# Kernel optimization log

Measured on AMD Instinct MI355X. Metric: run time of the kernel, lower is better.

## Reference

```python
import jax, jax.numpy as jnp
import numpy as np

B, S, N = 16, 512, 8          # batch, sentence length, num hash functions
M_BLOOM = 4096                # bloom filter length
W_WIN = 2                     # moving-window half width


def setup_inputs() -> dict:
    key = jax.random.key(0)
    hashes = jax.random.randint(key, (B, S, N), 0, 2147483647, dtype=jnp.int32)
    return {"hashes": hashes}


def counting_bloom(hashes, m):
    # hashes: [B, S, N] int -> counts [B, M, S] float32 (per-position histogram of N hashes mod m)
    b, s, _ = hashes.shape
    fp = jnp.remainder(hashes, m)
    counts = jnp.zeros((b, s, m), jnp.float32).at[
        jnp.arange(b)[:, None, None], jnp.arange(s)[None, :, None], fp
    ].add(1.0)
    return jnp.transpose(counts, (0, 2, 1))  # [B, M, S]


def moving_window(fc, w):
    # fc: [B, M, S] -> [B, (2w+1)*M, S]; block k holds fc shifted right by (w-k) along S, zero-padded
    _, _, s = fc.shape
    blocks = []
    for k in range(2 * w + 1):
        sh = w - k  # positive = shift right, negative = shift left
        if sh > 0:
            blk = jnp.pad(fc[:, :, : s - sh], ((0, 0), (0, 0), (sh, 0)))
        elif sh < 0:
            blk = jnp.pad(fc[:, :, -sh:], ((0, 0), (0, 0), (0, -sh)))
        else:
            blk = fc
        blocks.append(blk)
    return jnp.concatenate(blocks, axis=1)


def reference(hashes):
    fc = counting_bloom(hashes, M_BLOOM)      # [B, M, S]
    return moving_window(fc, W_WIN)           # [B, (2W+1)*M, S]
```

## Files before the change

kernel.cpp:

```cpp
#include <hip/hip_runtime.h>

#define B_DIM 16
#define S_DIM 512
#define N_HASH 8
#define M_BLOOM 4096
#define W_WIN 2
#define K_BLOCKS (2 * W_WIN + 1)
#define OUT_ELEMS (B_DIM * K_BLOCKS * M_BLOOM * S_DIM)

typedef float fx4 __attribute__((ext_vector_type(4)));

__global__ void zero_out_kernel(fx4* __restrict__ out, int n4) {
    const fx4 z = {0.0f, 0.0f, 0.0f, 0.0f};
    int idx = blockIdx.x * blockDim.x + threadIdx.x;
    const int stride = gridDim.x * blockDim.x;
    for (int i = idx; i < n4; i += stride) {
        out[i] = z;
    }
}

__global__ void scatter_kernel(const int* __restrict__ hashes,
                               float* __restrict__ out) {
    int idx = blockIdx.x * blockDim.x + threadIdx.x;
    if (idx >= B_DIM * S_DIM * N_HASH) return;

    const int b = idx / (S_DIM * N_HASH);
    const int s = (idx / N_HASH) % S_DIM;

    const int h = hashes[idx];
    const int m = h & (M_BLOOM - 1);

    const long long base_bm = ((long long)b * K_BLOCKS) * M_BLOOM + m;
#pragma unroll
    for (int k = 0; k < K_BLOCKS; ++k) {
        const int s_out = s + (W_WIN - k);
        if (s_out >= 0 && s_out < S_DIM) {
            const long long off =
                (base_bm + (long long)k * M_BLOOM) * S_DIM + s_out;
            atomicAdd(out + off, 1.0f);
        }
    }
}

extern "C" void kernel_launch(void* const* d_in, const int* in_sizes, int n_in,
                              void* d_out, int out_size, void* d_ws, size_t ws_size,
                              hipStream_t stream) {
    const int* hashes = (const int*)d_in[0];
    float* out = (float*)d_out;

    const int n4 = OUT_ELEMS / 4;
    zero_out_kernel<<<8192, 256, 0, stream>>>((fx4*)out, n4);

    const int total_hashes = B_DIM * S_DIM * N_HASH;
    scatter_kernel<<<(total_hashes + 255) / 256, 256, 0, stream>>>(hashes, out);
}
```

Before: 706.3 us.

## Fuse zeroing and atomic scatter into LDS histogram tile with dense shifted writes

Replaces the separate zero-fill kernel and the global atomicAdd scatter with one kernel. Each block owns one batch and a 64-row slice of the bloom dimension. It builds byte-sized counts in a padded LDS tile, then writes all five shifted window blocks as dense, coalesced float4 stores. This removes the extra full-output write pass and the scattered global atomics. In exchange, every block rereads the batch's hashes and does unaligned byte-extraction work in LDS.

```diff
diff --git a/kernel.cpp b/kernel.cpp
--- a/kernel.cpp
+++ b/kernel.cpp
@@ -1,4 +1,5 @@
 #include <hip/hip_runtime.h>
+#include <stdint.h>
 
 #define B_DIM 16
 #define S_DIM 512
@@ -8,37 +9,67 @@
 #define K_BLOCKS (2 * W_WIN + 1)
 #define OUT_ELEMS (B_DIM * K_BLOCKS * M_BLOOM * S_DIM)
 
+#define M_CHUNK 64
+#define TILE_STRIDE 520
+#define TILE_BYTES (M_CHUNK * TILE_STRIDE)
+
 typedef float fx4 __attribute__((ext_vector_type(4)));
 
-__global__ void zero_out_kernel(fx4* __restrict__ out, int n4) {
-    const fx4 z = {0.0f, 0.0f, 0.0f, 0.0f};
-    int idx = blockIdx.x * blockDim.x + threadIdx.x;
-    const int stride = gridDim.x * blockDim.x;
-    for (int i = idx; i < n4; i += stride) {
-        out[i] = z;
+__global__ __launch_bounds__(256) void bloom_window_kernel(
+    const int* __restrict__ hashes, float* __restrict__ out) {
+    __shared__ uint32_t tile32[TILE_BYTES / 4];
+    uint8_t* tile = (uint8_t*)tile32;
+
+    const int tid = threadIdx.x;
+    const int b = blockIdx.x >> 6;
+    const int chunk = blockIdx.x & 63;
+    const int m0 = chunk * M_CHUNK;
+
+    for (int i = tid; i < TILE_BYTES / 4; i += 256) tile32[i] = 0;
+    __syncthreads();
+
+    const int4* hp = (const int4*)hashes;
+#pragma unroll
+    for (int ss = 0; ss < 2; ++ss) {
+        const int s = 2 * tid + ss;
+        const int4 h01 = hp[(b * S_DIM + s) * 2 + 0];
+        const int4 h23 = hp[(b * S_DIM + s) * 2 + 1];
+        const int hv[8] = {h01.x, h01.y, h01.z, h01.w,
+                           h23.x, h23.y, h23.z, h23.w};
+#pragma unroll
+        for (int n = 0; n < N_HASH; ++n) {
+            const int m = hv[n] & (M_BLOOM - 1);
+            const unsigned ml = (unsigned)(m - m0);
+            if (ml < M_CHUNK) {
+                tile[ml * TILE_STRIDE + 4 + s] += 1;
+            }
+        }
     }
-}
+    __syncthreads();
 
-__global__ void scatter_kernel(const int* __restrict__ hashes,
-                               float* __restrict__ out) {
-    int idx = blockIdx.x * blockDim.x + threadIdx.x;
-    if (idx >= B_DIM * S_DIM * N_HASH) return;
+    fx4* out4 = (fx4*)out;
+    const int n_items = K_BLOCKS * M_CHUNK * (S_DIM / 4);
+    for (int idx = tid; idx < n_items; idx += 256) {
+        const int j = idx & 127;
+        const int r = idx >> 7;
+        const int k = r >> 6;
+        const int m = r & 63;
 
-    const int b = idx / (S_DIM * N_HASH);
-    const int s = (idx / N_HASH) % S_DIM;
+        const int base = m * TILE_STRIDE + 4 + 4 * j + (k - 2);
+        const uint32_t* wp = (const uint32_t*)(tile + (base & ~3));
+        const uint32_t lo = wp[0];
+        const uint32_t hi = wp[1];
+        const uint32_t sh = (uint32_t)(base & 3) * 8u;
+        const uint32_t packed = sh ? ((lo >> sh) | (hi << (32u - sh))) : lo;
 
-    const int h = hashes[idx];
-    const int m = h & (M_BLOOM - 1);
+        fx4 v;
+        v.x = (float)(packed & 0xffu);
+        v.y = (float)((packed >> 8) & 0xffu);
+        v.z = (float)((packed >> 16) & 0xffu);
+        v.w = (float)((packed >> 24) & 0xffu);
 
-    const long long base_bm = ((long long)b * K_BLOCKS) * M_BLOOM + m;
-#pragma unroll
-    for (int k = 0; k < K_BLOCKS; ++k) {
-        const int s_out = s + (W_WIN - k);
-        if (s_out >= 0 && s_out < S_DIM) {
-            const long long off =
-                (base_bm + (long long)k * M_BLOOM) * S_DIM + s_out;
-            atomicAdd(out + off, 1.0f);
-        }
+        const int row = (b * K_BLOCKS + k) * M_BLOOM + m0 + m;
+        out4[(long long)row * (S_DIM / 4) + j] = v;
     }
 }
 
@@ -48,9 +79,5 @@
     const int* hashes = (const int*)d_in[0];
     float* out = (float*)d_out;
 
-    const int n4 = OUT_ELEMS / 4;
-    zero_out_kernel<<<8192, 256, 0, stream>>>((fx4*)out, n4);
-
-    const int total_hashes = B_DIM * S_DIM * N_HASH;
-    scatter_kernel<<<(total_hashes + 255) / 256, 256, 0, stream>>>(hashes, out);
+    bloom_window_kernel<<<B_DIM * (M_BLOOM / M_CHUNK), 256, 0, stream>>>(hashes, out);
 }
```

Result: faster. 656.0 us (-7.1%).
